# Performance work log

Measured on AMD Instinct MI355X. Metric: run time of the kernel, lower is better.

## Reference

```python
import jax, jax.numpy as jnp
import numpy as np

EMBED_DIM = 131
SCALE = jnp.sqrt(jnp.float32(131.0))


def setup_inputs() -> dict:
    key = jax.random.key(0)
    ks = jax.random.split(key, 9)
    B, N, D = 8, 2048, EMBED_DIM
    s = 1.0 / np.sqrt(D)  # torch Linear default init scale (uniform bound)
    return {
        "query": jax.random.normal(ks[0], (B, N, D), dtype=jnp.float32),
        "key": jax.random.normal(ks[1], (B, N, D), dtype=jnp.float32),
        "value": jax.random.normal(ks[2], (B, N, D), dtype=jnp.float32),
        "Wq": jax.random.uniform(ks[3], (D, D), jnp.float32, -s, s),
        "bq": jax.random.uniform(ks[4], (D,), jnp.float32, -s, s),
        "Wk": jax.random.uniform(ks[5], (D, D), jnp.float32, -s, s),
        "bk": jax.random.uniform(ks[6], (D,), jnp.float32, -s, s),
        "Wv": jax.random.uniform(ks[7], (D, D), jnp.float32, -s, s),
        "bv": jax.random.uniform(ks[8], (D,), jnp.float32, -s, s),
    }


def reference(query, key, value, Wq, bq, Wk, bk, Wv, bv):
    # Linear projections (torch Linear: x @ W.T + b)
    Q = jnp.einsum("bnd,ed->bne", query, Wq) + bq  # [B, N, D]
    K = jnp.einsum("bnd,ed->bne", key, Wk) + bk    # [B, N, D]
    V = jnp.einsum("bnd,ed->bne", value, Wv) + bv  # [B, N, D]
    # Full attention with hardcoded scale sqrt(131)
    scores = jnp.einsum("bqd,bkd->bqk", Q, K) / SCALE  # [B, N, N]
    weights = jax.nn.softmax(scores, axis=-1)
    return jnp.einsum("bqk,bkd->bqd", weights, V)  # [B, N, D]
```

## Files before the change

### kernel.cpp

```cpp
#include <hip/hip_runtime.h>

#define B_ 8
#define N_ 2048
#define D_ 131
#define BN (B_ * N_)
#define KB 32
#define DT 9
#define PSTR 40
#define COSTR 145
#define SXSTR 164
#define CSTR 168
#define TSTR 72

typedef __attribute__((ext_vector_type(8))) short s16x8;
typedef __attribute__((ext_vector_type(4))) float f32x4;

__device__ __forceinline__ ushort f2bf(float x) {
  uint u = __float_as_uint(x);
  u += 0x7fffu + ((u >> 16) & 1u);
  return (ushort)(u >> 16);
}
__device__ __forceinline__ float bf2f(ushort h) {
  return __uint_as_float(((uint)h) << 16);
}
__device__ __forceinline__ uint bfpair(float a, float b) {
  uint ua = __float_as_uint(a);
  ua += 0x7fffu + ((ua >> 16) & 1u);
  uint ub = __float_as_uint(b);
  ub += 0x7fffu + ((ub >> 16) & 1u);
  return (ua >> 16) | (ub & 0xffff0000u);
}

__device__ __forceinline__ size_t rf_idx(int nt, int ch, int l) {
  return (((size_t)nt * 5 + ch) * 64 + l) * 8;
}
__device__ __forceinline__ size_t vf_idx(int ktg, int dt, int l) {
  return (((size_t)ktg * 9 + dt) * 64 + l) * 8;
}
__device__ __forceinline__ size_t wf_idx(int p, int h, int et, int ch, int l) {
  return (((((size_t)p * 2 + h) * 9 + et) * 5 + ch) * 64 + l) * 8;
}

__global__ void cast_w_kernel(const float* __restrict__ Wq,
                              const float* __restrict__ Wk,
                              const float* __restrict__ Wv,
                              ushort* __restrict__ Whl) {
  const int p = blockIdx.x;
  const float* __restrict__ W = (p == 0) ? Wq : (p == 1) ? Wk : Wv;
  for (int i = threadIdx.x; i < 9 * 5 * 64; i += blockDim.x) {
    const int et = i / 320;
    const int rem = i - et * 320;
    const int ch = rem >> 6;
    const int l = rem & 63;
    const int lr = l & 15, lg = l >> 4;
    const int e = et * 16 + lr;
    s16x8 hi, lo;
#pragma unroll
    for (int j = 0; j < 8; ++j) {
      const int d = ch * 32 + lg * 8 + j;
      const float val = (e < D_ && d < D_) ? W[e * D_ + d] : 0.f;
      const ushort h = f2bf(val);
      hi[j] = (short)h;
      lo[j] = (short)f2bf(val - bf2f(h));
    }
    *(s16x8*)(Whl + wf_idx(p, 0, et, ch, l)) = hi;
    *(s16x8*)(Whl + wf_idx(p, 1, et, ch, l)) = lo;
  }
}

__global__ __launch_bounds__(256, 3) void proj_gemm(
    const float* __restrict__ q, const float* __restrict__ k,
    const float* __restrict__ v, const float* __restrict__ bq,
    const float* __restrict__ bk, const float* __restrict__ bv,
    const ushort* __restrict__ Whl, ushort* __restrict__ Qf,
    ushort* __restrict__ Kf, ushort* __restrict__ Vf) {
  const int p = blockIdx.y;
  const float* __restrict__ x = (p == 0) ? q : (p == 1) ? k : v;
  const float* __restrict__ bias = (p == 0) ? bq : (p == 1) ? bk : bv;

  __shared__ __align__(16) char smem[64 * SXSTR * 4];
  float* sX = (float*)smem;
  ushort* sC = (ushort*)smem;
  ushort* sT = (ushort*)smem;
  __shared__ float sB[160];

  const int tid = threadIdx.x;
  const int r0 = blockIdx.x * 64;

  for (int i = tid; i < 64 * SXSTR; i += 256) {
    const int r = i / SXSTR;
    const int d = i - r * SXSTR;
    sX[i] = (d < D_) ? x[(size_t)(r0 + r) * D_ + d] : 0.f;
  }
  if (tid < 160) sB[tid] = (tid < D_) ? bias[tid] : 0.f;
  __syncthreads();

  const int w = tid >> 6;
  const int l = tid & 63;
  const int lr = l & 15;
  const int lg = l >> 4;

  f32x4 acc[9];
#pragma unroll
  for (int et = 0; et < 9; ++et) acc[et] = (f32x4){0.f, 0.f, 0.f, 0.f};

#pragma unroll
  for (int ch = 0; ch < 5; ++ch) {
    const float* xp = sX + (size_t)(w * 16 + lr) * SXSTR + ch * 32 + lg * 8;
    const float4 x0 = *(const float4*)xp;
    const float4 x1 = *(const float4*)(xp + 4);
    const float xv[8] = {x0.x, x0.y, x0.z, x0.w, x1.x, x1.y, x1.z, x1.w};
    s16x8 ah, al;
#pragma unroll
    for (int j = 0; j < 8; ++j) {
      const ushort h = f2bf(xv[j]);
      ah[j] = (short)h;
      al[j] = (short)f2bf(xv[j] - bf2f(h));
    }
#pragma unroll
    for (int et = 0; et < 9; ++et) {
      const s16x8 bh = *(const s16x8*)(Whl + wf_idx(p, 0, et, ch, l));
      const s16x8 bl = *(const s16x8*)(Whl + wf_idx(p, 1, et, ch, l));
      acc[et] = __builtin_amdgcn_mfma_f32_16x16x32_bf16(ah, bh, acc[et], 0, 0, 0);
      acc[et] = __builtin_amdgcn_mfma_f32_16x16x32_bf16(al, bh, acc[et], 0, 0, 0);
      acc[et] = __builtin_amdgcn_mfma_f32_16x16x32_bf16(ah, bl, acc[et], 0, 0, 0);
    }
  }

  const float ISC = 0.08737040566610379f;
  __syncthreads();

  if (p < 2) {
#pragma unroll
    for (int et = 0; et < 9; ++et) {
      const int e = et * 16 + lr;
      const float bval = sB[e];
#pragma unroll
      for (int r = 0; r < 4; ++r) {
        float val = acc[et][r] + bval;
        if (p == 0) val *= ISC;
        sC[(size_t)(w * 16 + lg * 4 + r) * CSTR + e] = f2bf(val);
      }
    }
    for (int i = tid; i < 64 * 16; i += 256)
      sC[(size_t)(i >> 4) * CSTR + 144 + (i & 15)] = 0;
    __syncthreads();
    ushort* __restrict__ dst = (p == 0) ? Qf : Kf;
    const int nt0 = r0 >> 4;
    for (int i = tid; i < 4 * 5 * 64; i += 256) {
      const int nt = i / 320;
      const int rem = i - nt * 320;
      const int ch = rem >> 6;
      const int l2 = rem & 63;
      const s16x8 fr = *(const s16x8*)(sC + (size_t)(nt * 16 + (l2 & 15)) * CSTR +
                                       ch * 32 + (l2 >> 4) * 8);
      *(s16x8*)(dst + rf_idx(nt0 + nt, ch, l2)) = fr;
    }
  } else {
    for (int i = tid; i < 13 * 64; i += 256) {
      const int e = D_ + (i >> 6);
      sT[(size_t)e * TSTR + (i & 63)] = (e == D_) ? (ushort)0x3F80 : (ushort)0;
    }
#pragma unroll
    for (int et = 0; et < 9; ++et) {
      const int e = et * 16 + lr;
      if (e < D_) {
        const float bval = sB[e];
#pragma unroll
        for (int r = 0; r < 4; ++r)
          sT[(size_t)e * TSTR + w * 16 + lg * 4 + r] = f2bf(acc[et][r] + bval);
      }
    }
    __syncthreads();
    const int kt0 = r0 >> 5;
    for (int i = tid; i < 2 * 9 * 64; i += 256) {
      const int ktl = i / 576;
      const int rem = i - ktl * 576;
      const int dt = rem >> 6;
      const int l2 = rem & 63;
      const s16x8 fr = *(const s16x8*)(sT + (size_t)(dt * 16 + (l2 & 15)) * TSTR +
                                       ktl * 32 + (l2 >> 4) * 8);
      *(s16x8*)(Vf + vf_idx(kt0 + ktl, dt, l2)) = fr;
    }
  }
}

__global__ __launch_bounds__(256, 2) void attn_mfma(
    const ushort* __restrict__ Qf, const ushort* __restrict__ Kf,
    const ushort* __restrict__ Vf, float* __restrict__ out) {
  const int id = blockIdx.x;
  const int b = id & 7;
  const int q0 = (id >> 3) * 32;
  const int tid = threadIdx.x;
  const int w = tid >> 6;
  const int l = tid & 63;
  const int lr = l & 15;
  const int lg = l >> 4;

  __shared__ ushort sP[4][32 * PSTR];
  __shared__ float cm[3][32];
  __shared__ float cO[3][32][COSTR];

  ushort* sPw = sP[w];
  const int qnt0 = b * 128 + (q0 >> 4);

  s16x8 qf[2][5];
#pragma unroll
  for (int qt = 0; qt < 2; ++qt)
#pragma unroll
    for (int ch = 0; ch < 5; ++ch)
      qf[qt][ch] = *(const s16x8*)(Qf + rf_idx(qnt0 + qt, ch, l));

  s16x8 kA[2][5], kB[2][5];
  {
    const int knt = b * 128 + w * 32;
#pragma unroll
    for (int ch = 0; ch < 5; ++ch)
#pragma unroll
      for (int a = 0; a < 2; ++a)
        kA[a][ch] = *(const s16x8*)(Kf + rf_idx(knt + a, ch, l));
  }

  f32x4 o[2][DT];
#pragma unroll
  for (int qt = 0; qt < 2; ++qt)
#pragma unroll
    for (int dt = 0; dt < DT; ++dt) o[qt][dt] = (f32x4){0.f, 0.f, 0.f, 0.f};
  float mreg[2] = {-1e30f, -1e30f};

  auto tile_body = [&](s16x8(&KC)[2][5], s16x8(&KN)[2][5], int kt, int ktn) {
    s16x8 vf[DT];
#pragma unroll
    for (int dt = 0; dt < DT; ++dt)
      vf[dt] = *(const s16x8*)(Vf + vf_idx(b * 64 + kt, dt, l));
    {
      const int knt = b * 128 + ktn * 2;
#pragma unroll
      for (int ch = 0; ch < 5; ++ch)
#pragma unroll
        for (int a = 0; a < 2; ++a)
          KN[a][ch] = *(const s16x8*)(Kf + rf_idx(knt + a, ch, l));
    }
    f32x4 s[2][2];
#pragma unroll
    for (int a = 0; a < 2; ++a)
#pragma unroll
      for (int qt = 0; qt < 2; ++qt) s[a][qt] = (f32x4){0.f, 0.f, 0.f, 0.f};
#pragma unroll
    for (int ch = 0; ch < 5; ++ch) {
      s[0][0] = __builtin_amdgcn_mfma_f32_16x16x32_bf16(KC[0][ch], qf[0][ch], s[0][0], 0, 0, 0);
      s[1][0] = __builtin_amdgcn_mfma_f32_16x16x32_bf16(KC[1][ch], qf[0][ch], s[1][0], 0, 0, 0);
      s[0][1] = __builtin_amdgcn_mfma_f32_16x16x32_bf16(KC[0][ch], qf[1][ch], s[0][1], 0, 0, 0);
      s[1][1] = __builtin_amdgcn_mfma_f32_16x16x32_bf16(KC[1][ch], qf[1][ch], s[1][1], 0, 0, 0);
    }
#pragma unroll
    for (int qt = 0; qt < 2; ++qt) {
      float tm = s[0][qt][0];
#pragma unroll
      for (int a = 0; a < 2; ++a)
#pragma unroll
        for (int r = 0; r < 4; ++r) tm = fmaxf(tm, s[a][qt][r]);
      tm = fmaxf(tm, __shfl_xor(tm, 16, 64));
      tm = fmaxf(tm, __shfl_xor(tm, 32, 64));
      if (__any(tm > mreg[qt])) {
        const float mo = mreg[qt];
        const float mn = fmaxf(mo, tm);
        mreg[qt] = mn;
        const float f = __expf(mo - mn);
        float fr[4];
#pragma unroll
        for (int r = 0; r < 4; ++r) fr[r] = __shfl(f, lg * 4 + r, 64);
#pragma unroll
        for (int dt = 0; dt < DT; ++dt)
#pragma unroll
          for (int r = 0; r < 4; ++r) o[qt][dt][r] *= fr[r];
      }
      const float mcur = mreg[qt];
#pragma unroll
      for (int a = 0; a < 2; ++a) {
        const float p0 = __expf(s[a][qt][0] - mcur);
        const float p1 = __expf(s[a][qt][1] - mcur);
        const float p2 = __expf(s[a][qt][2] - mcur);
        const float p3 = __expf(s[a][qt][3] - mcur);
        uint2 u;
        u.x = bfpair(p0, p1);
        u.y = bfpair(p2, p3);
        *(uint2*)(sPw + (size_t)(qt * 16 + lr) * PSTR + a * 16 + lg * 4) = u;
      }
    }
    const s16x8 pa0 = *(const s16x8*)(sPw + (size_t)lr * PSTR + lg * 8);
    const s16x8 pa1 = *(const s16x8*)(sPw + (size_t)(16 + lr) * PSTR + lg * 8);
#pragma unroll
    for (int dt = 0; dt < DT; ++dt) {
      o[0][dt] = __builtin_amdgcn_mfma_f32_16x16x32_bf16(pa0, vf[dt], o[0][dt], 0, 0, 0);
      o[1][dt] = __builtin_amdgcn_mfma_f32_16x16x32_bf16(pa1, vf[dt], o[1][dt], 0, 0, 0);
    }
  };

  for (int i = 0; i < 8; ++i) {
    const int kt = w * 16 + 2 * i;
    tile_body(kA, kB, kt, kt + 1);
    tile_body(kB, kA, kt + 1, (i < 7) ? kt + 2 : kt + 1);
  }

  if (w > 0) {
    if (lg == 0) {
      cm[w - 1][lr] = mreg[0];
      cm[w - 1][16 + lr] = mreg[1];
    }
#pragma unroll
    for (int qt = 0; qt < 2; ++qt)
#pragma unroll
      for (int dt = 0; dt < DT; ++dt)
#pragma unroll
        for (int r = 0; r < 4; ++r)
          cO[w - 1][qt * 16 + lg * 4 + r][dt * 16 + lr] = o[qt][dt][r];
  }
  __syncthreads();
  if (w == 0) {
#pragma unroll
    for (int qt = 0; qt < 2; ++qt) {
      const int qq = qt * 16 + lr;
      const float m1 = cm[0][qq], m2 = cm[1][qq], m3 = cm[2][qq];
      const float M = fmaxf(fmaxf(mreg[qt], m1), fmaxf(m2, m3));
      const float e0 = __expf(mreg[qt] - M);
      const float e1 = __expf(m1 - M);
      const float e2 = __expf(m2 - M);
      const float e3 = __expf(m3 - M);
      float er0[4], er1[4], er2[4], er3[4];
#pragma unroll
      for (int r = 0; r < 4; ++r) {
        er0[r] = __shfl(e0, lg * 4 + r, 64);
        er1[r] = __shfl(e1, lg * 4 + r, 64);
        er2[r] = __shfl(e2, lg * 4 + r, 64);
        er3[r] = __shfl(e3, lg * 4 + r, 64);
      }
      float l8[4];
#pragma unroll
      for (int r = 0; r < 4; ++r) {
        const int row = qt * 16 + lg * 4 + r;
        l8[r] = o[qt][8][r] * er0[r] + cO[0][row][128 + lr] * er1[r] +
                cO[1][row][128 + lr] * er2[r] + cO[2][row][128 + lr] * er3[r];
      }
      float ir[4];
#pragma unroll
      for (int r = 0; r < 4; ++r)
        ir[r] = 1.f / __shfl(l8[r], (l & 48) + 3, 64);
#pragma unroll
      for (int dt = 0; dt < DT; ++dt) {
        const int d = dt * 16 + lr;
        if (d < D_) {
#pragma unroll
          for (int r = 0; r < 4; ++r) {
            const int row = qt * 16 + lg * 4 + r;
            const float val = (dt == 8 ? l8[r]
                                       : o[qt][dt][r] * er0[r] +
                                             cO[0][row][d] * er1[r] +
                                             cO[1][row][d] * er2[r] +
                                             cO[2][row][d] * er3[r]);
            out[((size_t)b * N_ + q0 + row) * D_ + d] = val * ir[r];
          }
        }
      }
    }
  }
}

extern "C" void kernel_launch(void* const* d_in, const int* in_sizes, int n_in,
                              void* d_out, int out_size, void* d_ws,
                              size_t ws_size, hipStream_t stream) {
  const float* q = (const float*)d_in[0];
  const float* k = (const float*)d_in[1];
  const float* v = (const float*)d_in[2];
  const float* Wq = (const float*)d_in[3];
  const float* bq = (const float*)d_in[4];
  const float* Wk = (const float*)d_in[5];
  const float* bk = (const float*)d_in[6];
  const float* Wv = (const float*)d_in[7];
  const float* bv = (const float*)d_in[8];
  float* out = (float*)d_out;

  char* wsb = (char*)d_ws;
  ushort* Qf = (ushort*)(wsb);
  ushort* Kf = (ushort*)(wsb + 5242880);
  ushort* Vf = (ushort*)(wsb + 10485760);
  ushort* Whl = (ushort*)(wsb + 15204352);

  hipLaunchKernelGGL(cast_w_kernel, dim3(3), dim3(256), 0, stream, Wq, Wk, Wv,
                     Whl);
  hipLaunchKernelGGL(proj_gemm, dim3(256, 3), dim3(256), 0, stream, q, k, v,
                     bq, bk, bv, Whl, Qf, Kf, Vf);
  hipLaunchKernelGGL(attn_mfma, dim3(512), dim3(256), 0, stream, Qf, Kf, Vf,
                     out);
}
```

Baseline: 81.39 us.

## Double query tile per attention block, stage Q in LDS, vectorize projection loads

The attention kernel now handles 64 query rows per block instead of 32, halving the grid so each loaded K/V tile is reused across four query subtiles. Q fragments are staged in shared memory, and the cross-wave merge is rewritten so all four waves cooperate on the final combine in two 32-row chunks with row-contiguous output writes. The projection kernel loads input rows with float4 and batches weight-fragment loads in groups of three. The cost is more accumulator registers (occupancy hint lowered to 1 block per CU) and only 256 blocks on a large GPU, which risks underutilizing compute units.

Measured after the change: 90.72 us. 11.5% more time.

```diff
diff --git a/kernel.cpp b/kernel.cpp
--- a/kernel.cpp
+++ b/kernel.cpp
@@ -87,10 +87,23 @@
   const int tid = threadIdx.x;
   const int r0 = blockIdx.x * 64;
 
-  for (int i = tid; i < 64 * SXSTR; i += 256) {
-    const int r = i / SXSTR;
-    const int d = i - r * SXSTR;
-    sX[i] = (d < D_) ? x[(size_t)(r0 + r) * D_ + d] : 0.f;
+  {
+    const float* __restrict__ xbase = x + (size_t)r0 * D_;
+    for (int i = tid; i < 64 * D_ / 4; i += 256) {
+      const float4 v4 = *(const float4*)(xbase + i * 4);
+      const float vv[4] = {v4.x, v4.y, v4.z, v4.w};
+#pragma unroll
+      for (int j = 0; j < 4; ++j) {
+        const int nl = i * 4 + j;
+        const int r = nl / D_;
+        const int d = nl - r * D_;
+        sX[r * SXSTR + d] = vv[j];
+      }
+    }
+    for (int i = tid; i < 64 * 33; i += 256) {
+      const int r = i / 33;
+      sX[r * SXSTR + D_ + (i - r * 33)] = 0.f;
+    }
   }
   if (tid < 160) sB[tid] = (tid < D_) ? bias[tid] : 0.f;
   __syncthreads();
@@ -118,12 +131,20 @@
       al[j] = (short)f2bf(xv[j] - bf2f(h));
     }
 #pragma unroll
-    for (int et = 0; et < 9; ++et) {
-      const s16x8 bh = *(const s16x8*)(Whl + wf_idx(p, 0, et, ch, l));
-      const s16x8 bl = *(const s16x8*)(Whl + wf_idx(p, 1, et, ch, l));
-      acc[et] = __builtin_amdgcn_mfma_f32_16x16x32_bf16(ah, bh, acc[et], 0, 0, 0);
-      acc[et] = __builtin_amdgcn_mfma_f32_16x16x32_bf16(al, bh, acc[et], 0, 0, 0);
-      acc[et] = __builtin_amdgcn_mfma_f32_16x16x32_bf16(ah, bl, acc[et], 0, 0, 0);
+    for (int eg = 0; eg < 3; ++eg) {
+      s16x8 bh[3], bl[3];
+#pragma unroll
+      for (int u = 0; u < 3; ++u) {
+        bh[u] = *(const s16x8*)(Whl + wf_idx(p, 0, eg * 3 + u, ch, l));
+        bl[u] = *(const s16x8*)(Whl + wf_idx(p, 1, eg * 3 + u, ch, l));
+      }
+#pragma unroll
+      for (int u = 0; u < 3; ++u) {
+        const int et = eg * 3 + u;
+        acc[et] = __builtin_amdgcn_mfma_f32_16x16x32_bf16(ah, bh[u], acc[et], 0, 0, 0);
+        acc[et] = __builtin_amdgcn_mfma_f32_16x16x32_bf16(al, bh[u], acc[et], 0, 0, 0);
+        acc[et] = __builtin_amdgcn_mfma_f32_16x16x32_bf16(ah, bl[u], acc[et], 0, 0, 0);
+      }
     }
   }
 
@@ -185,31 +206,31 @@
   }
 }
 
-__global__ __launch_bounds__(256, 2) void attn_mfma(
+__global__ __launch_bounds__(256, 1) void attn_mfma(
     const ushort* __restrict__ Qf, const ushort* __restrict__ Kf,
     const ushort* __restrict__ Vf, float* __restrict__ out) {
   const int id = blockIdx.x;
   const int b = id & 7;
-  const int q0 = (id >> 3) * 32;
+  const int q0 = (id >> 3) * 64;
   const int tid = threadIdx.x;
   const int w = tid >> 6;
   const int l = tid & 63;
   const int lr = l & 15;
   const int lg = l >> 4;
 
-  __shared__ ushort sP[4][32 * PSTR];
-  __shared__ float cm[3][32];
-  __shared__ float cO[3][32][COSTR];
+  __shared__ ushort sQ[4 * 5 * 64 * 8];
+  __shared__ ushort sP[4][64 * PSTR];
+  __shared__ float cO[4][32][COSTR];
+  __shared__ float cm[4][32];
 
   ushort* sPw = sP[w];
-  const int qnt0 = b * 128 + (q0 >> 4);
-
-  s16x8 qf[2][5];
-#pragma unroll
-  for (int qt = 0; qt < 2; ++qt)
-#pragma unroll
-    for (int ch = 0; ch < 5; ++ch)
-      qf[qt][ch] = *(const s16x8*)(Qf + rf_idx(qnt0 + qt, ch, l));
+
+  {
+    const uint4* src =
+        (const uint4*)(Qf + rf_idx(b * 128 + (q0 >> 4), 0, 0));
+    uint4* dst = (uint4*)sQ;
+    for (int i = tid; i < 4 * 5 * 64; i += 256) dst[i] = src[i];
+  }
 
   s16x8 kA[2][5], kB[2][5];
   {
@@ -220,13 +241,14 @@
       for (int a = 0; a < 2; ++a)
         kA[a][ch] = *(const s16x8*)(Kf + rf_idx(knt + a, ch, l));
   }
-
-  f32x4 o[2][DT];
-#pragma unroll
-  for (int qt = 0; qt < 2; ++qt)
+  __syncthreads();
+
+  f32x4 o[4][DT];
+#pragma unroll
+  for (int qt = 0; qt < 4; ++qt)
 #pragma unroll
     for (int dt = 0; dt < DT; ++dt) o[qt][dt] = (f32x4){0.f, 0.f, 0.f, 0.f};
-  float mreg[2] = {-1e30f, -1e30f};
+  float mreg[4] = {-1e30f, -1e30f, -1e30f, -1e30f};
 
   auto tile_body = [&](s16x8(&KC)[2][5], s16x8(&KN)[2][5], int kt, int ktn) {
     s16x8 vf[DT];
@@ -241,25 +263,19 @@
         for (int a = 0; a < 2; ++a)
           KN[a][ch] = *(const s16x8*)(Kf + rf_idx(knt + a, ch, l));
     }
-    f32x4 s[2][2];
-#pragma unroll
-    for (int a = 0; a < 2; ++a)
-#pragma unroll
-      for (int qt = 0; qt < 2; ++qt) s[a][qt] = (f32x4){0.f, 0.f, 0.f, 0.f};
-#pragma unroll
-    for (int ch = 0; ch < 5; ++ch) {
-      s[0][0] = __builtin_amdgcn_mfma_f32_16x16x32_bf16(KC[0][ch], qf[0][ch], s[0][0], 0, 0, 0);
-      s[1][0] = __builtin_amdgcn_mfma_f32_16x16x32_bf16(KC[1][ch], qf[0][ch], s[1][0], 0, 0, 0);
-      s[0][1] = __builtin_amdgcn_mfma_f32_16x16x32_bf16(KC[0][ch], qf[1][ch], s[0][1], 0, 0, 0);
-      s[1][1] = __builtin_amdgcn_mfma_f32_16x16x32_bf16(KC[1][ch], qf[1][ch], s[1][1], 0, 0, 0);
-    }
-#pragma unroll
-    for (int qt = 0; qt < 2; ++qt) {
-      float tm = s[0][qt][0];
-#pragma unroll
-      for (int a = 0; a < 2; ++a)
-#pragma unroll
-        for (int r = 0; r < 4; ++r) tm = fmaxf(tm, s[a][qt][r]);
+#pragma unroll
+    for (int qt = 0; qt < 4; ++qt) {
+      f32x4 s0 = (f32x4){0.f, 0.f, 0.f, 0.f};
+      f32x4 s1 = (f32x4){0.f, 0.f, 0.f, 0.f};
+#pragma unroll
+      for (int ch = 0; ch < 5; ++ch) {
+        const s16x8 qfc = *(const s16x8*)(sQ + ((qt * 5 + ch) * 64 + l) * 8);
+        s0 = __builtin_amdgcn_mfma_f32_16x16x32_bf16(KC[0][ch], qfc, s0, 0, 0, 0);
+        s1 = __builtin_amdgcn_mfma_f32_16x16x32_bf16(KC[1][ch], qfc, s1, 0, 0, 0);
+      }
+      float tm = s0[0];
+#pragma unroll
+      for (int r = 0; r < 4; ++r) tm = fmaxf(tm, fmaxf(s0[r], s1[r]));
       tm = fmaxf(tm, __shfl_xor(tm, 16, 64));
       tm = fmaxf(tm, __shfl_xor(tm, 32, 64));
       if (__any(tm > mreg[qt])) {
@@ -276,25 +292,34 @@
           for (int r = 0; r < 4; ++r) o[qt][dt][r] *= fr[r];
       }
       const float mcur = mreg[qt];
-#pragma unroll
-      for (int a = 0; a < 2; ++a) {
-        const float p0 = __expf(s[a][qt][0] - mcur);
-        const float p1 = __expf(s[a][qt][1] - mcur);
-        const float p2 = __expf(s[a][qt][2] - mcur);
-        const float p3 = __expf(s[a][qt][3] - mcur);
-        uint2 u;
-        u.x = bfpair(p0, p1);
-        u.y = bfpair(p2, p3);
-        *(uint2*)(sPw + (size_t)(qt * 16 + lr) * PSTR + a * 16 + lg * 4) = u;
-      }
-    }
-    const s16x8 pa0 = *(const s16x8*)(sPw + (size_t)lr * PSTR + lg * 8);
-    const s16x8 pa1 = *(const s16x8*)(sPw + (size_t)(16 + lr) * PSTR + lg * 8);
-#pragma unroll
-    for (int dt = 0; dt < DT; ++dt) {
-      o[0][dt] = __builtin_amdgcn_mfma_f32_16x16x32_bf16(pa0, vf[dt], o[0][dt], 0, 0, 0);
-      o[1][dt] = __builtin_amdgcn_mfma_f32_16x16x32_bf16(pa1, vf[dt], o[1][dt], 0, 0, 0);
-    }
+      {
+        const float p0 = __expf(s0[0] - mcur);
+        const float p1 = __expf(s0[1] - mcur);
+        const float p2 = __expf(s0[2] - mcur);
+        const float p3 = __expf(s0[3] - mcur);
+        const float p4 = __expf(s1[0] - mcur);
+        const float p5 = __expf(s1[1] - mcur);
+        const float p6 = __expf(s1[2] - mcur);
+        const float p7 = __expf(s1[3] - mcur);
+        uint2 u0, u1;
+        u0.x = bfpair(p0, p1);
+        u0.y = bfpair(p2, p3);
+        u1.x = bfpair(p4, p5);
+        u1.y = bfpair(p6, p7);
+        *(uint2*)(sPw + (size_t)(qt * 16 + lr) * PSTR + lg * 4) = u0;
+        *(uint2*)(sPw + (size_t)(qt * 16 + lr) * PSTR + 16 + lg * 4) = u1;
+      }
+    }
+    s16x8 pa[4];
+#pragma unroll
+    for (int qt = 0; qt < 4; ++qt)
+      pa[qt] = *(const s16x8*)(sPw + (size_t)(qt * 16 + lr) * PSTR + lg * 8);
+#pragma unroll
+    for (int dt = 0; dt < DT; ++dt)
+#pragma unroll
+      for (int qt = 0; qt < 4; ++qt)
+        o[qt][dt] =
+            __builtin_amdgcn_mfma_f32_16x16x32_bf16(pa[qt], vf[dt], o[qt][dt], 0, 0, 0);
   };
 
   for (int i = 0; i < 8; ++i) {
@@ -303,64 +328,40 @@
     tile_body(kB, kA, kt + 1, (i < 7) ? kt + 2 : kt + 1);
   }
 
-  if (w > 0) {
+#pragma unroll
+  for (int c = 0; c < 2; ++c) {
+    if (c) __syncthreads();
     if (lg == 0) {
-      cm[w - 1][lr] = mreg[0];
-      cm[w - 1][16 + lr] = mreg[1];
-    }
-#pragma unroll
-    for (int qt = 0; qt < 2; ++qt)
+#pragma unroll
+      for (int qq = 0; qq < 2; ++qq) cm[w][qq * 16 + lr] = mreg[c * 2 + qq];
+    }
+#pragma unroll
+    for (int qq = 0; qq < 2; ++qq) {
+      const int qt = c * 2 + qq;
 #pragma unroll
       for (int dt = 0; dt < DT; ++dt)
 #pragma unroll
         for (int r = 0; r < 4; ++r)
-          cO[w - 1][qt * 16 + lg * 4 + r][dt * 16 + lr] = o[qt][dt][r];
-  }
-  __syncthreads();
-  if (w == 0) {
-#pragma unroll
-    for (int qt = 0; qt < 2; ++qt) {
-      const int qq = qt * 16 + lr;
-      const float m1 = cm[0][qq], m2 = cm[1][qq], m3 = cm[2][qq];
-      const float M = fmaxf(fmaxf(mreg[qt], m1), fmaxf(m2, m3));
-      const float e0 = __expf(mreg[qt] - M);
+          cO[w][qq * 16 + lg * 4 + r][dt * 16 + lr] = o[qt][dt][r];
+    }
+    __syncthreads();
+    for (int rr = 0; rr < 8; ++rr) {
+      const int row = w * 8 + rr;
+      const float m0 = cm[0][row], m1 = cm[1][row];
+      const float m2 = cm[2][row], m3 = cm[3][row];
+      const float M = fmaxf(fmaxf(m0, m1), fmaxf(m2, m3));
+      const float e0 = __expf(m0 - M);
       const float e1 = __expf(m1 - M);
       const float e2 = __expf(m2 - M);
       const float e3 = __expf(m3 - M);
-      float er0[4], er1[4], er2[4], er3[4];
-#pragma unroll
-      for (int r = 0; r < 4; ++r) {
-        er0[r] = __shfl(e0, lg * 4 + r, 64);
-        er1[r] = __shfl(e1, lg * 4 + r, 64);
-        er2[r] = __shfl(e2, lg * 4 + r, 64);
-        er3[r] = __shfl(e3, lg * 4 + r, 64);
-      }
-      float l8[4];
-#pragma unroll
-      for (int r = 0; r < 4; ++r) {
-        const int row = qt * 16 + lg * 4 + r;
-        l8[r] = o[qt][8][r] * er0[r] + cO[0][row][128 + lr] * er1[r] +
-                cO[1][row][128 + lr] * er2[r] + cO[2][row][128 + lr] * er3[r];
-      }
-      float ir[4];
-#pragma unroll
-      for (int r = 0; r < 4; ++r)
-        ir[r] = 1.f / __shfl(l8[r], (l & 48) + 3, 64);
-#pragma unroll
-      for (int dt = 0; dt < DT; ++dt) {
-        const int d = dt * 16 + lr;
-        if (d < D_) {
-#pragma unroll
-          for (int r = 0; r < 4; ++r) {
-            const int row = qt * 16 + lg * 4 + r;
-            const float val = (dt == 8 ? l8[r]
-                                       : o[qt][dt][r] * er0[r] +
-                                             cO[0][row][d] * er1[r] +
-                                             cO[1][row][d] * er2[r] +
-                                             cO[2][row][d] * er3[r]);
-            out[((size_t)b * N_ + q0 + row) * D_ + d] = val * ir[r];
-          }
-        }
+      const float lsum = cO[0][row][D_] * e0 + cO[1][row][D_] * e1 +
+                         cO[2][row][D_] * e2 + cO[3][row][D_] * e3;
+      const float inv = 1.f / lsum;
+      float* orow = out + ((size_t)b * N_ + q0 + c * 32 + row) * D_;
+      for (int d = l; d < D_; d += 64) {
+        const float val = cO[0][row][d] * e0 + cO[1][row][d] * e1 +
+                          cO[2][row][d] * e2 + cO[3][row][d] * e3;
+        orow[d] = val * inv;
       }
     }
   }
@@ -390,6 +391,6 @@
                      Whl);
   hipLaunchKernelGGL(proj_gemm, dim3(256, 3), dim3(256), 0, stream, q, k, v,
                      bq, bk, bv, Whl, Qf, Kf, Vf);
-  hipLaunchKernelGGL(attn_mfma, dim3(512), dim3(256), 0, stream, Qf, Kf, Vf,
+  hipLaunchKernelGGL(attn_mfma, dim3(256), dim3(256), 0, stream, Qf, Kf, Vf,
                      out);
 }
```
